# Kernel optimization log

Measured on AMD Instinct MI355X. Metric: run time of the kernel, lower is better.

## Reference

```python
import jax, jax.numpy as jnp
import numpy as np

BS, N, D, H = 4, 2048, 512, 8
DK = D // H
XAVIER_STD = float(np.sqrt(2.0 / (D + D)))  # xavier_normal_, gain=1


def setup_inputs() -> dict:
    key = jax.random.key(0)
    ks = jax.random.split(key, 10)
    Q = jax.random.normal(ks[0], (BS, N, D), jnp.float32)
    K = jax.random.normal(ks[1], (BS, N, D), jnp.float32)
    V = jax.random.normal(ks[2], (BS, N, D), jnp.float32)
    q_mas = jax.random.randint(ks[3], (BS, N, 1), 0, 2).astype(jnp.float32)
    k_mas = jax.random.randint(ks[4], (BS, N, 1), 0, 2).astype(jnp.float32)
    # 0/1 attention mask; force self-edges so no row is fully masked (avoids NaN softmax)
    att_mas = jax.random.randint(ks[5], (BS, N, N), 0, 2).astype(jnp.float32)
    att_mas = jnp.maximum(att_mas, jnp.eye(N, dtype=jnp.float32)[None])
    WQ = jax.random.normal(ks[6], (D, D), jnp.float32) * XAVIER_STD
    WK = jax.random.normal(ks[7], (D, D), jnp.float32) * XAVIER_STD
    WV = jax.random.normal(ks[8], (D, D), jnp.float32) * XAVIER_STD
    WO = jax.random.normal(ks[9], (D, D), jnp.float32) * XAVIER_STD
    return {"Q": Q, "K": K, "V": V, "q_mas": q_mas, "k_mas": k_mas,
            "att_mas": att_mas, "WQ": WQ, "WK": WK, "WV": WV, "WO": WO}


def reference(Q, K, V, q_mas, k_mas, att_mas, WQ, WK, WV, WO):
    bs, n, d = Q.shape
    h, dk = H, DK
    qm = q_mas.reshape(bs, 1, n, 1)  # (bs,1,n,1)
    km = k_mas.reshape(bs, 1, n, 1)
    # nn.Linear (no bias): x @ W.T ; split heads -> (bs,h,n,dk); apply pre-masks
    Qh = qm * (Q @ WQ.T).reshape(bs, n, h, dk).transpose(0, 2, 1, 3)
    Kh = km * (K @ WK.T).reshape(bs, n, h, dk).transpose(0, 2, 1, 3)
    Vh = km * (V @ WV.T).reshape(bs, n, h, dk).transpose(0, 2, 1, 3)
    scores = jnp.einsum('bhqd,bhkd->bhqk', Qh, Kh) / jnp.sqrt(jnp.float32(dk))
    mas = att_mas.reshape(bs, 1, n, n)
    scores = jnp.where(mas.astype(bool), scores, -jnp.inf)
    attn = jax.nn.softmax(scores, axis=-1) * mas
    y = jnp.einsum('bhqk,bhkd->bhqd', attn, Vh) * km  # post-mask (note: km over query dim, as in source)
    y = y.transpose(0, 2, 1, 3).reshape(bs, n, d)
    y = (y @ WO.T) * k_mas.reshape(bs, n, 1)
    return y
```

## Files before the change

kernel.cpp:

```cpp
#include <hip/hip_runtime.h>


#define BS_    4
#define NSEQ   2048
#define DMODEL 512
#define NH     8
#define DKH    64
#define MROWS  (BS_ * NSEQ)

typedef unsigned short ushort_t;
typedef __attribute__((ext_vector_type(8))) short short8;
typedef __attribute__((ext_vector_type(4))) float floatx4;

__device__ __forceinline__ ushort_t f2bf(float f) {
    unsigned int x = __builtin_bit_cast(unsigned int, f);
    return (ushort_t)((x + 0x8000u) >> 16);
}
__device__ __forceinline__ floatx4 mfma_bf16(short8 a, short8 b, floatx4 c) {
    return __builtin_amdgcn_mfma_f32_16x16x32_bf16(a, b, c, 0, 0, 0);
}
__device__ __forceinline__ void gld16(const ushort_t* g, ushort_t* l) {
    __builtin_amdgcn_global_load_lds(
        (const __attribute__((address_space(1))) unsigned int*)g,
        (__attribute__((address_space(3))) unsigned int*)l, 16, 0, 0);
}

__global__ __launch_bounds__(256) void cvt3_kernel(const float* __restrict__ a,
                                                   const float* __restrict__ b,
                                                   const float* __restrict__ c,
                                                   ushort_t* __restrict__ dst, int n4) {
    const float* src = (blockIdx.y == 0) ? a : (blockIdx.y == 1) ? b : c;
    ushort_t* d = dst + (size_t)blockIdx.y * ((size_t)n4 * 4);
    const int i = blockIdx.x * blockDim.x + threadIdx.x;
    const float4 v = ((const float4*)src)[i];
    ushort4 o;
    o.x = f2bf(v.x); o.y = f2bf(v.y); o.z = f2bf(v.z); o.w = f2bf(v.w);
    ((ushort4*)d)[i] = o;
}

__global__ __launch_bounds__(256) void cvt4_kernel(const float* __restrict__ a,
                                                   const float* __restrict__ b,
                                                   const float* __restrict__ c,
                                                   const float* __restrict__ e,
                                                   ushort_t* __restrict__ dst, int n4) {
    const float* src = (blockIdx.y == 0) ? a : (blockIdx.y == 1) ? b
                     : (blockIdx.y == 2) ? c : e;
    ushort_t* d = dst + (size_t)blockIdx.y * ((size_t)n4 * 4);
    const int i = blockIdx.x * blockDim.x + threadIdx.x;
    const float4 v = ((const float4*)src)[i];
    ushort4 o;
    o.x = f2bf(v.x); o.y = f2bf(v.y); o.z = f2bf(v.z); o.w = f2bf(v.w);
    ((ushort4*)d)[i] = o;
}

__global__ __launch_bounds__(256) void gemm_proj(const ushort_t* __restrict__ Xall,
                                                 const ushort_t* __restrict__ Wall,
                                                 const float* __restrict__ qmas,
                                                 const float* __restrict__ kmas,
                                                 ushort_t* __restrict__ Qh,
                                                 ushort_t* __restrict__ Kh,
                                                 ushort_t* __restrict__ Vt) {
    __shared__ ushort_t As[2][128 * 32];
    const int z = blockIdx.z;
    const ushort_t* X  = Xall + (size_t)z * MROWS * DMODEL;
    const ushort_t* Wb = Wall + (size_t)z * DMODEL * DMODEL;
    const float* rowmask = (z == 0) ? qmas : kmas;

    const int tid  = threadIdx.x;
    const int wave = tid >> 6;
    const int lane = tid & 63;
    const int l16  = lane & 15;
    const int quad = lane >> 4;
    const int wr   = wave >> 1;
    const int wc   = wave & 1;
    const int m0   = blockIdx.x * 128;
    const int n0   = blockIdx.y * 128;
    const int r4   = lane >> 2;
    const int p4   = lane & 3;

    floatx4 acc[4][4];
#pragma unroll
    for (int t = 0; t < 4; ++t)
#pragma unroll
        for (int u = 0; u < 4; ++u) acc[t][u] = (floatx4){0.f, 0.f, 0.f, 0.f};

    const ushort_t* Wrow[4];
#pragma unroll
    for (int u = 0; u < 4; ++u)
        Wrow[u] = Wb + (size_t)(n0 + wc * 64 + u * 16 + l16) * DMODEL + quad * 8;

    for (int k0 = 0; k0 < DMODEL; k0 += 64) {
#pragma unroll
        for (int i = 0; i < 4; ++i) {
            const int idx = wave * 4 + i;
            const int h = idx >> 3, rg = idx & 7;
            gld16(X + (size_t)(m0 + rg * 16 + r4) * DMODEL + k0 + h * 32 + p4 * 8,
                  &As[h][rg * 512]);
        }
        short8 bf[4][2];
#pragma unroll
        for (int u = 0; u < 4; ++u)
#pragma unroll
            for (int kc = 0; kc < 2; ++kc)
                bf[u][kc] = *(const short8*)(Wrow[u] + k0 + kc * 32);
        __syncthreads();
        short8 af[4][2];
#pragma unroll
        for (int t = 0; t < 4; ++t)
#pragma unroll
            for (int kc = 0; kc < 2; ++kc)
                af[t][kc] = *(const short8*)&As[kc][(wr * 64 + t * 16 + l16) * 32 + quad * 8];
#pragma unroll
        for (int t = 0; t < 4; ++t)
#pragma unroll
            for (int u = 0; u < 4; ++u) {
                acc[t][u] = mfma_bf16(af[t][0], bf[u][0], acc[t][u]);
                acc[t][u] = mfma_bf16(af[t][1], bf[u][1], acc[t][u]);
            }
        __syncthreads();
    }

    float rm[4][4];
#pragma unroll
    for (int t = 0; t < 4; ++t)
#pragma unroll
        for (int r = 0; r < 4; ++r)
            rm[t][r] = rowmask[m0 + wr * 64 + t * 16 + quad * 4 + r];

    const int bb    = m0 >> 11;
    const int nbase = (m0 & (NSEQ - 1)) + wr * 64;
#pragma unroll
    for (int t = 0; t < 4; ++t) {
#pragma unroll
        for (int u = 0; u < 4; ++u) {
            const int d = n0 + wc * 64 + u * 16 + l16;
            const int h = d >> 6, cc = d & 63;
            if (z < 2) {
                ushort_t* dst = (z == 0) ? Qh : Kh;
#pragma unroll
                for (int r = 0; r < 4; ++r) {
                    const int n = nbase + t * 16 + quad * 4 + r;
                    dst[((size_t)(bb * NH + h) * NSEQ + n) * DKH + cc] =
                        f2bf(acc[t][u][r] * rm[t][r]);
                }
            } else {
                ushort4 pk;
                pk.x = f2bf(acc[t][u][0] * rm[t][0]);
                pk.y = f2bf(acc[t][u][1] * rm[t][1]);
                pk.z = f2bf(acc[t][u][2] * rm[t][2]);
                pk.w = f2bf(acc[t][u][3] * rm[t][3]);
                const int n = nbase + t * 16 + quad * 4;
                *(ushort4*)(Vt + ((size_t)(bb * NH + h) * DKH + cc) * NSEQ + n) = pk;
            }
        }
    }
}

__global__ __launch_bounds__(256) void gemm_out(const ushort_t* __restrict__ X,
                                                const ushort_t* __restrict__ Wb,
                                                const float* __restrict__ rowmask,
                                                float* __restrict__ dst) {
    __shared__ ushort_t As[2][128 * 32];
    const int tid  = threadIdx.x;
    const int wave = tid >> 6;
    const int lane = tid & 63;
    const int l16  = lane & 15;
    const int quad = lane >> 4;
    const int wr   = wave >> 1;
    const int wc   = wave & 1;
    const int m0   = blockIdx.x * 128;
    const int n0   = blockIdx.y * 128;
    const int r4   = lane >> 2;
    const int p4   = lane & 3;

    floatx4 acc[4][4];
#pragma unroll
    for (int t = 0; t < 4; ++t)
#pragma unroll
        for (int u = 0; u < 4; ++u) acc[t][u] = (floatx4){0.f, 0.f, 0.f, 0.f};

    const ushort_t* Wrow[4];
#pragma unroll
    for (int u = 0; u < 4; ++u)
        Wrow[u] = Wb + (size_t)(n0 + wc * 64 + u * 16 + l16) * DMODEL + quad * 8;

    for (int k0 = 0; k0 < DMODEL; k0 += 64) {
#pragma unroll
        for (int i = 0; i < 4; ++i) {
            const int idx = wave * 4 + i;
            const int h = idx >> 3, rg = idx & 7;
            gld16(X + (size_t)(m0 + rg * 16 + r4) * DMODEL + k0 + h * 32 + p4 * 8,
                  &As[h][rg * 512]);
        }
        short8 bf[4][2];
#pragma unroll
        for (int u = 0; u < 4; ++u)
#pragma unroll
            for (int kc = 0; kc < 2; ++kc)
                bf[u][kc] = *(const short8*)(Wrow[u] + k0 + kc * 32);
        __syncthreads();
        short8 af[4][2];
#pragma unroll
        for (int t = 0; t < 4; ++t)
#pragma unroll
            for (int kc = 0; kc < 2; ++kc)
                af[t][kc] = *(const short8*)&As[kc][(wr * 64 + t * 16 + l16) * 32 + quad * 8];
#pragma unroll
        for (int t = 0; t < 4; ++t)
#pragma unroll
            for (int u = 0; u < 4; ++u) {
                acc[t][u] = mfma_bf16(af[t][0], bf[u][0], acc[t][u]);
                acc[t][u] = mfma_bf16(af[t][1], bf[u][1], acc[t][u]);
            }
        __syncthreads();
    }

#pragma unroll
    for (int t = 0; t < 4; ++t) {
#pragma unroll
        for (int r = 0; r < 4; ++r) {
            const int m = m0 + wr * 64 + t * 16 + quad * 4 + r;
            const float rm = rowmask[m];
#pragma unroll
            for (int u = 0; u < 4; ++u) {
                const int d = n0 + wc * 64 + u * 16 + l16;
                dst[(size_t)m * DMODEL + d] = acc[t][u][r] * rm;
            }
        }
    }
}

__global__ __launch_bounds__(256, 3) void attn_kernel(const ushort_t* __restrict__ Qh,
                                                      const ushort_t* __restrict__ Kh,
                                                      const ushort_t* __restrict__ Vt,
                                                      const float* __restrict__ amas,
                                                      const float* __restrict__ kmas,
                                                      ushort_t* __restrict__ y) {
    __shared__ ushort_t Ks[2][128 * 32];
    __shared__ ushort_t Vs[4][64 * 32];
    __shared__ ushort_t Ps[4][4][16 * 32];

    const int tid  = threadIdx.x;
    const int wave = tid >> 6;
    const int lane = tid & 63;
    const int l16  = lane & 15;
    const int quad = lane >> 4;
    const int r4   = lane >> 2;
    const int p4   = lane & 3;
    const int h    = blockIdx.y;
    const int b    = blockIdx.z;
    const int qw   = blockIdx.x * 64 + wave * 16;

    const ushort_t* Kb = Kh + (size_t)(b * NH + h) * NSEQ * DKH;
    const ushort_t* Vb = Vt + (size_t)(b * NH + h) * DKH * NSEQ;
    const float*    Am = amas + (size_t)(b * NSEQ + qw) * NSEQ;

    const ushort_t* Qp = Qh + ((size_t)((b * NH + h) * NSEQ) + qw + l16) * DKH + quad * 8;
    const short8 qfa = *(const short8*)Qp;
    const short8 qfb = *(const short8*)(Qp + 32);

    float lpart[4] = {0.f, 0.f, 0.f, 0.f};
    floatx4 accO[4];
#pragma unroll
    for (int ct = 0; ct < 4; ++ct) accO[ct] = (floatx4){0.f, 0.f, 0.f, 0.f};

    const float CEXP = 0.18033688011112042f;

    for (int kt = 0; kt < NSEQ / 128; ++kt) {
        const int k0 = kt * 128;

        __syncthreads();

        float av[8][4];
#pragma unroll
        for (int fr = 0; fr < 8; ++fr)
#pragma unroll
            for (int r = 0; r < 4; ++r)
                av[fr][r] = Am[(size_t)(quad * 4 + r) * NSEQ + k0 + fr * 16 + l16];

#pragma unroll
        for (int i = 0; i < 4; ++i) {
            const int idx = wave * 4 + i;
            const int hh = idx >> 3, rg = idx & 7;
            gld16(Kb + (size_t)(k0 + rg * 16 + r4) * DKH + hh * 32 + p4 * 8,
                  &Ks[hh][rg * 512]);
        }
#pragma unroll
        for (int i = 0; i < 4; ++i) {
            const int idx = wave * 4 + i;
            const int kf = idx >> 2, rg = idx & 3;
            gld16(Vb + (size_t)(rg * 16 + r4) * NSEQ + k0 + kf * 32 + p4 * 8,
                  &Vs[kf][rg * 512]);
        }
        __syncthreads();

        floatx4 S[8];
#pragma unroll
        for (int fr = 0; fr < 8; ++fr) {
            const short8 ka = *(const short8*)&Ks[0][(fr * 16 + l16) * 32 + quad * 8];
            const short8 kb = *(const short8*)&Ks[1][(fr * 16 + l16) * 32 + quad * 8];
            floatx4 s = {0.f, 0.f, 0.f, 0.f};
            s = mfma_bf16(qfa, ka, s);
            s = mfma_bf16(qfb, kb, s);
            S[fr] = s;
        }

#pragma unroll
        for (int fr = 0; fr < 8; ++fr) {
#pragma unroll
            for (int r = 0; r < 4; ++r) {
                const float p = av[fr][r] * exp2f(S[fr][r] * CEXP);
                lpart[r] += p;
                Ps[wave][fr >> 1][(quad * 4 + r) * 32 + (fr & 1) * 16 + l16] = f2bf(p);
            }
        }

        __builtin_amdgcn_wave_barrier();
        short8 pf[4];
#pragma unroll
        for (int kf = 0; kf < 4; ++kf)
            pf[kf] = *(const short8*)&Ps[wave][kf][l16 * 32 + quad * 8];
        __builtin_amdgcn_wave_barrier();

#pragma unroll
        for (int ct = 0; ct < 4; ++ct) {
#pragma unroll
            for (int kf = 0; kf < 4; ++kf) {
                const short8 vb = *(const short8*)&Vs[kf][(ct * 16 + l16) * 32 + quad * 8];
                accO[ct] = mfma_bf16(pf[kf], vb, accO[ct]);
            }
        }
    }

#pragma unroll
    for (int r = 0; r < 4; ++r) {
        float l = lpart[r];
        l += __shfl_xor(l, 1);
        l += __shfl_xor(l, 2);
        l += __shfl_xor(l, 4);
        l += __shfl_xor(l, 8);
        const int q = qw + quad * 4 + r;
        const float scale = kmas[b * NSEQ + q] / l;
#pragma unroll
        for (int ct = 0; ct < 4; ++ct) {
            y[(size_t)(b * NSEQ + q) * DMODEL + h * DKH + ct * 16 + l16] =
                f2bf(accO[ct][r] * scale);
        }
    }
}

extern "C" void kernel_launch(void* const* d_in, const int* in_sizes, int n_in,
                              void* d_out, int out_size, void* d_ws, size_t ws_size,
                              hipStream_t stream) {
    (void)in_sizes; (void)n_in; (void)out_size; (void)ws_size;
    const float* Q  = (const float*)d_in[0];
    const float* K  = (const float*)d_in[1];
    const float* V  = (const float*)d_in[2];
    const float* qm = (const float*)d_in[3];
    const float* km = (const float*)d_in[4];
    const float* am = (const float*)d_in[5];
    const float* WQ = (const float*)d_in[6];
    const float* WK = (const float*)d_in[7];
    const float* WV = (const float*)d_in[8];
    const float* WO = (const float*)d_in[9];

    const size_t XN = (size_t)MROWS * DMODEL;
    const size_t WN = (size_t)DMODEL * DMODEL;
    ushort_t* Xbf = (ushort_t*)d_ws;
    ushort_t* Wbf = Xbf + 3 * XN;
    ushort_t* WOb = Wbf + 3 * WN;
    ushort_t* Qh  = Wbf + 4 * WN;
    ushort_t* Kh  = Qh + XN;
    ushort_t* Vt  = Kh + XN;
    ushort_t* y   = Vt + XN;
    float* out = (float*)d_out;

    hipLaunchKernelGGL(cvt3_kernel, dim3(4096, 3), dim3(256), 0, stream,
                       Q, K, V, Xbf, (int)(XN / 4));
    hipLaunchKernelGGL(cvt4_kernel, dim3(256, 4), dim3(256), 0, stream,
                       WQ, WK, WV, WO, Wbf, (int)(WN / 4));

    hipLaunchKernelGGL(gemm_proj, dim3(MROWS / 128, DMODEL / 128, 3), dim3(256), 0, stream,
                       Xbf, Wbf, qm, km, Qh, Kh, Vt);

    hipLaunchKernelGGL(attn_kernel, dim3(NSEQ / 64, NH, BS_), dim3(256), 0, stream,
                       Qh, Kh, Vt, am, km, y);

    hipLaunchKernelGGL(gemm_out, dim3(MROWS / 128, DMODEL / 128), dim3(256), 0, stream,
                       y, WOb, km, out);
}
```

Before: 294.2 us.

## Pack attention mask to bitmask once and stage Q/K stores through LDS

Adds a pre-pass that packs the float attention mask into one bit per entry using wave ballots. The attention kernel then reads compact mask words instead of float values, so the eight heads no longer each re-read the 64 MB float mask. The Q/K projection epilogue also stages each wave's tile in shared memory so it can write full 16-byte rows instead of scattered 2-byte stores. The cost is one extra full pass over the float mask plus a small workspace buffer, and per-element bit extraction in the softmax loop.

```diff
diff --git a/kernel.cpp b/kernel.cpp
--- a/kernel.cpp
+++ b/kernel.cpp
@@ -7,6 +7,7 @@
 #define NH     8
 #define DKH    64
 #define MROWS  (BS_ * NSEQ)
+#define NW32   (NSEQ / 32)
 
 typedef unsigned short ushort_t;
 typedef __attribute__((ext_vector_type(8))) short short8;
@@ -23,6 +24,17 @@
     __builtin_amdgcn_global_load_lds(
         (const __attribute__((address_space(1))) unsigned int*)g,
         (__attribute__((address_space(3))) unsigned int*)l, 16, 0, 0);
+}
+
+__global__ __launch_bounds__(256) void pack_mask(const float* __restrict__ am,
+                                                 unsigned int* __restrict__ pm) {
+    const int gid = blockIdx.x * 256 + threadIdx.x;
+    const float v = am[gid];
+    const unsigned long long m = __ballot(v != 0.f);
+    if ((threadIdx.x & 63) == 0) {
+        uint2 w; w.x = (unsigned int)m; w.y = (unsigned int)(m >> 32);
+        *(uint2*)&pm[gid >> 5] = w;
+    }
 }
 
 __global__ __launch_bounds__(256) void cvt3_kernel(const float* __restrict__ a,
@@ -129,21 +141,37 @@
 
     const int bb    = m0 >> 11;
     const int nbase = (m0 & (NSEQ - 1)) + wr * 64;
-#pragma unroll
-    for (int t = 0; t < 4; ++t) {
-#pragma unroll
-        for (int u = 0; u < 4; ++u) {
-            const int d = n0 + wc * 64 + u * 16 + l16;
-            const int h = d >> 6, cc = d & 63;
-            if (z < 2) {
-                ushort_t* dst = (z == 0) ? Qh : Kh;
-#pragma unroll
-                for (int r = 0; r < 4; ++r) {
-                    const int n = nbase + t * 16 + quad * 4 + r;
-                    dst[((size_t)(bb * NH + h) * NSEQ + n) * DKH + cc] =
+
+    if (z < 2) {
+        ushort_t* patch = (ushort_t*)As + wave * 1152;
+        ushort_t* dst = (z == 0) ? Qh : Kh;
+        const int hh = (n0 >> 6) + wc;
+        const int rl = lane >> 2;
+        const int cb = (lane & 3) * 16;
+#pragma unroll
+        for (int t = 0; t < 4; ++t) {
+#pragma unroll
+            for (int u = 0; u < 4; ++u)
+#pragma unroll
+                for (int r = 0; r < 4; ++r)
+                    patch[(quad * 4 + r) * 72 + u * 16 + l16] =
                         f2bf(acc[t][u][r] * rm[t][r]);
-                }
-            } else {
+            __builtin_amdgcn_wave_barrier();
+            const int n = nbase + t * 16 + rl;
+            ushort_t* drow = dst + ((size_t)(bb * NH + hh) * NSEQ + n) * DKH;
+#pragma unroll
+            for (int c_ = 0; c_ < 2; ++c_)
+                *(short8*)&drow[cb + c_ * 8] =
+                    *(const short8*)&patch[rl * 72 + cb + c_ * 8];
+            __builtin_amdgcn_wave_barrier();
+        }
+    } else {
+#pragma unroll
+        for (int t = 0; t < 4; ++t) {
+#pragma unroll
+            for (int u = 0; u < 4; ++u) {
+                const int d = n0 + wc * 64 + u * 16 + l16;
+                const int h = d >> 6, cc = d & 63;
                 ushort4 pk;
                 pk.x = f2bf(acc[t][u][0] * rm[t][0]);
                 pk.y = f2bf(acc[t][u][1] * rm[t][1]);
@@ -233,7 +261,7 @@
 __global__ __launch_bounds__(256, 3) void attn_kernel(const ushort_t* __restrict__ Qh,
                                                       const ushort_t* __restrict__ Kh,
                                                       const ushort_t* __restrict__ Vt,
-                                                      const float* __restrict__ amas,
+                                                      const unsigned int* __restrict__ pmask,
                                                       const float* __restrict__ kmas,
                                                       ushort_t* __restrict__ y) {
     __shared__ ushort_t Ks[2][128 * 32];
@@ -253,7 +281,7 @@
 
     const ushort_t* Kb = Kh + (size_t)(b * NH + h) * NSEQ * DKH;
     const ushort_t* Vb = Vt + (size_t)(b * NH + h) * DKH * NSEQ;
-    const float*    Am = amas + (size_t)(b * NSEQ + qw) * NSEQ;
+    const unsigned int* Pm = pmask + (size_t)(b * NSEQ + qw) * NW32;
 
     const ushort_t* Qp = Qh + ((size_t)((b * NH + h) * NSEQ) + qw + l16) * DKH + quad * 8;
     const short8 qfa = *(const short8*)Qp;
@@ -271,12 +299,12 @@
 
         __syncthreads();
 
-        float av[8][4];
-#pragma unroll
-        for (int fr = 0; fr < 8; ++fr)
-#pragma unroll
-            for (int r = 0; r < 4; ++r)
-                av[fr][r] = Am[(size_t)(quad * 4 + r) * NSEQ + k0 + fr * 16 + l16];
+        unsigned int mw[4][4];
+#pragma unroll
+        for (int r = 0; r < 4; ++r) {
+            const uint4 m4 = *(const uint4*)&Pm[(size_t)(quad * 4 + r) * NW32 + kt * 4];
+            mw[r][0] = m4.x; mw[r][1] = m4.y; mw[r][2] = m4.z; mw[r][3] = m4.w;
+        }
 
 #pragma unroll
         for (int i = 0; i < 4; ++i) {
@@ -309,7 +337,9 @@
         for (int fr = 0; fr < 8; ++fr) {
 #pragma unroll
             for (int r = 0; r < 4; ++r) {
-                const float p = av[fr][r] * exp2f(S[fr][r] * CEXP);
+                const unsigned int bit = (mw[r][fr >> 1] >> ((fr & 1) * 16 + l16)) & 1u;
+                const float e = exp2f(S[fr][r] * CEXP);
+                const float p = bit ? e : 0.f;
                 lpart[r] += p;
                 Ps[wave][fr >> 1][(quad * 4 + r) * 32 + (fr & 1) * 16 + l16] = f2bf(p);
             }
@@ -373,8 +403,11 @@
     ushort_t* Kh  = Qh + XN;
     ushort_t* Vt  = Kh + XN;
     ushort_t* y   = Vt + XN;
+    unsigned int* pm = (unsigned int*)(y + XN);
     float* out = (float*)d_out;
 
+    hipLaunchKernelGGL(pack_mask, dim3((BS_ * NSEQ * NSEQ) / 256), dim3(256), 0, stream,
+                       am, pm);
     hipLaunchKernelGGL(cvt3_kernel, dim3(4096, 3), dim3(256), 0, stream,
                        Q, K, V, Xbf, (int)(XN / 4));
     hipLaunchKernelGGL(cvt4_kernel, dim3(256, 4), dim3(256), 0, stream,
@@ -384,7 +417,7 @@
                        Xbf, Wbf, qm, km, Qh, Kh, Vt);
 
     hipLaunchKernelGGL(attn_kernel, dim3(NSEQ / 64, NH, BS_), dim3(256), 0, stream,
-                       Qh, Kh, Vt, am, km, y);
+                       Qh, Kh, Vt, pm, km, y);
 
     hipLaunchKernelGGL(gemm_out, dim3(MROWS / 128, DMODEL / 128), dim3(256), 0, stream,
                        y, WOb, km, out);
```

Result: slower. 320.9 us (+9.1%).
